# Optimization experiments

Hardware: AMD Instinct MI355X
Metric: run time of the kernel (lower is better)

## Reference

```python
import jax, jax.numpy as jnp
import numpy as np

N_SLOTS = 524288
DIM_MEM = 128
DIM_IN = 1024
SHIFT_RADIUS = 3
EPS = 1e-8  # torch cosine_similarity eps


def setup_inputs() -> dict:
    key = jax.random.key(0)
    k1, k2, k3, k4, k5 = jax.random.split(key, 5)
    n_factors = DIM_MEM + 1 + 1 + (2 * SHIFT_RADIUS + 1) + 1  # 138
    return {
        "input_from_controller": jax.random.normal(k1, (DIM_IN,), dtype=jnp.float32),
        "previous_weighting": jax.random.uniform(k2, (N_SLOTS,), dtype=jnp.float32),
        "memory": jax.random.normal(k3, (N_SLOTS, DIM_MEM), dtype=jnp.float32),
        "W_wf": jax.random.normal(k4, (DIM_IN, n_factors), dtype=jnp.float32) * 0.02,
        "b_wf": jax.random.normal(k5, (n_factors,), dtype=jnp.float32) * 0.02,
    }


def _get_weighting(input_from_controller, previous_weighting, memory, W_wf, b_wf):
    factors = input_from_controller @ W_wf + b_wf  # [138]
    M = DIM_MEM
    key_v = factors[:M]                       # [M]
    key_s = factors[M]                        # scalar (beta)
    gate = jax.nn.softmax(factors[M + 1:M + 2])      # size-1 softmax -> 1.0 (faithful)
    shift_w = jax.nn.softmax(factors[M + 2:M + 2 + 2 * SHIFT_RADIUS + 1])  # [2r+1]
    sharpening = jax.nn.relu(factors[-1]) + 1.0

    # content addressing: cosine similarity of each memory row with key_v
    mem_norm = jnp.maximum(jnp.linalg.norm(memory, axis=1), EPS)  # [N]
    key_norm = jnp.maximum(jnp.linalg.norm(key_v), EPS)
    content_w = (memory @ key_v) / (mem_norm * key_norm)          # [N]
    content_w = jax.nn.softmax(key_s * content_w)

    gated_w = content_w * gate[0] + (1.0 - gate[0]) * previous_weighting

    # circular convolution: shifted[i] = sum_j gated[(i - r + j) % N] * shift_w[j]
    shifted_w = jnp.zeros_like(gated_w)
    for j in range(2 * SHIFT_RADIUS + 1):  # small fixed tap count (7)
        shifted_w = shifted_w + shift_w[j] * jnp.roll(gated_w, SHIFT_RADIUS - j)

    pw = shifted_w ** sharpening
    return pw / pw.sum()


def reference(input_from_controller, previous_weighting, memory, W_wf, b_wf):
    w = _get_weighting(input_from_controller, previous_weighting, memory, W_wf, b_wf)
    read_vector = w @ memory  # read head forward
    return read_vector
```

## Files before the change

kernel.cpp:

```cpp
#include <hip/hip_runtime.h>
#include <math.h>

#define N_SLOTS 524288
#define DIM_MEM 128
#define DIM_IN 1024
#define NFACT 138
#define EPSF 1e-8f


__global__ __launch_bounds__(256) void k_factors(const float* __restrict__ x,
                                                 const float* __restrict__ W,
                                                 const float* __restrict__ b,
                                                 float* __restrict__ factors) {
    int j = threadIdx.x;
    int i0 = blockIdx.x * 32;
    if (j < NFACT) {
        float acc = 0.f;
        #pragma unroll 8
        for (int i = i0; i < i0 + 32; ++i)
            acc = fmaf(x[i], W[(size_t)i * NFACT + j], acc);
        if (blockIdx.x == 0) acc += b[j];
        atomicAdd(&factors[j], acc);
    }
}

__global__ void k_derived(const float* __restrict__ f, float* __restrict__ d) {
    int l = threadIdx.x;
    float v = f[l] * f[l] + f[l + 64] * f[l + 64];
    for (int off = 32; off; off >>= 1) v += __shfl_xor(v, off, 64);
    if (l == 0) {
        float key_norm = fmaxf(sqrtf(v), EPSF);
        float key_s = f[128];
        d[0] = key_s / key_norm;
        float m = f[130];
        for (int j = 1; j < 7; ++j) m = fmaxf(m, f[130 + j]);
        float e[7], s = 0.f;
        for (int j = 0; j < 7; ++j) { e[j] = expf(f[130 + j] - m); s += e[j]; }
        for (int j = 0; j < 7; ++j) d[1 + j] = e[j] / s;
        d[8] = fmaxf(f[137], 0.f) + 1.f;
    }
}

__global__ __launch_bounds__(256) void k_content(const float* __restrict__ mem,
                                                 const float* __restrict__ keyv,
                                                 const float* __restrict__ der,
                                                 float* __restrict__ e_out,
                                                 double* __restrict__ S_acc) {
    __shared__ float s_sum;
    if (threadIdx.x == 0) s_sum = 0.f;
    __syncthreads();
    const int lane = threadIdx.x & 31;
    const int hw   = threadIdx.x >> 5;
    const float4 k4 = ((const float4*)keyv)[lane];
    const float d0 = der[0];
    float local = 0.f;
    const int stride = gridDim.x * 8;
    for (int r = blockIdx.x * 8 + hw; r < N_SLOTS; r += stride) {
        float4 m4 = ((const float4*)(mem + (size_t)r * DIM_MEM))[lane];
        float dot = m4.x * k4.x + m4.y * k4.y + m4.z * k4.z + m4.w * k4.w;
        float n2  = m4.x * m4.x + m4.y * m4.y + m4.z * m4.z + m4.w * m4.w;
        for (int off = 16; off; off >>= 1) {
            dot += __shfl_xor(dot, off, 32);
            n2  += __shfl_xor(n2,  off, 32);
        }
        if (lane == 0) {
            float score = d0 * dot / fmaxf(sqrtf(n2), EPSF);
            float e = expf(score);
            e_out[r] = e;
            local += e;
        }
    }
    if (lane == 0) atomicAdd(&s_sum, local);
    __syncthreads();
    if (threadIdx.x == 0) atomicAdd(S_acc, (double)s_sum);
}

__global__ __launch_bounds__(256) void k_shift(const float* __restrict__ e,
                                               const float* __restrict__ der,
                                               const double* __restrict__ S_acc,
                                               float* __restrict__ p_out,
                                               double* __restrict__ P_acc) {
    __shared__ float s_sum;
    if (threadIdx.x == 0) s_sum = 0.f;
    __syncthreads();
    const int i = blockIdx.x * blockDim.x + threadIdx.x;
    const float invS = (float)(1.0 / *S_acc);
    const float sh = der[8];
    float t = 0.f;
    #pragma unroll
    for (int d = 0; d < 7; ++d) {
        int idx = i + d - 3;
        if (idx < 0) idx += N_SLOTS;
        if (idx >= N_SLOTS) idx -= N_SLOTS;
        t = fmaf(der[1 + d], e[idx], t);
    }
    float p = powf(t * invS, sh);
    p_out[i] = p;
    float w = p;
    for (int off = 32; off; off >>= 1) w += __shfl_xor(w, off, 64);
    if ((threadIdx.x & 63) == 0) atomicAdd(&s_sum, w);
    __syncthreads();
    if (threadIdx.x == 0) atomicAdd(P_acc, (double)s_sum);
}

__global__ __launch_bounds__(256) void k_read(const float* __restrict__ mem,
                                              const float* __restrict__ p,
                                              const double* __restrict__ P_acc,
                                              float* __restrict__ out) {
    __shared__ float partials[8][DIM_MEM];
    const int lane = threadIdx.x & 31;
    const int hw   = threadIdx.x >> 5;
    const float invP = (float)(1.0 / *P_acc);
    float4 acc = make_float4(0.f, 0.f, 0.f, 0.f);
    const int stride = gridDim.x * 8;
    for (int r = blockIdx.x * 8 + hw; r < N_SLOTS; r += stride) {
        float w = p[r] * invP;
        float4 m4 = ((const float4*)(mem + (size_t)r * DIM_MEM))[lane];
        acc.x = fmaf(w, m4.x, acc.x);
        acc.y = fmaf(w, m4.y, acc.y);
        acc.z = fmaf(w, m4.z, acc.z);
        acc.w = fmaf(w, m4.w, acc.w);
    }
    ((float4*)partials[hw])[lane] = acc;
    __syncthreads();
    if (threadIdx.x < DIM_MEM) {
        float s = 0.f;
        #pragma unroll
        for (int h = 0; h < 8; ++h) s += partials[h][threadIdx.x];
        atomicAdd(&out[threadIdx.x], s);
    }
}

extern "C" void kernel_launch(void* const* d_in, const int* in_sizes, int n_in,
                              void* d_out, int out_size, void* d_ws, size_t ws_size,
                              hipStream_t stream) {
    const float* x   = (const float*)d_in[0];
    const float* mem = (const float*)d_in[2];
    const float* W   = (const float*)d_in[3];
    const float* b   = (const float*)d_in[4];
    float* out = (float*)d_out;

    char* ws = (char*)d_ws;
    float*  factors = (float*)ws;
    float*  derived = (float*)(ws + 1024);
    double* S_acc   = (double*)(ws + 2048);
    double* P_acc   = (double*)(ws + 2056);
    float*  e_buf   = (float*)(ws + 4096);
    float*  p_buf   = (float*)(ws + 4096 + (size_t)N_SLOTS * 4);

    hipMemsetAsync(ws, 0, 4096, stream);
    hipMemsetAsync(d_out, 0, DIM_MEM * sizeof(float), stream);

    k_factors<<<DIM_IN / 32, 256, 0, stream>>>(x, W, b, factors);
    k_derived<<<1, 64, 0, stream>>>(factors, derived);
    k_content<<<1024, 256, 0, stream>>>(mem, factors, derived, e_buf, S_acc);
    k_shift<<<N_SLOTS / 256, 256, 0, stream>>>(e_buf, derived, S_acc, p_buf, P_acc);
    k_read<<<1024, 256, 0, stream>>>(mem, p_buf, P_acc, out);
}
```

Baseline: 459.2 us.

## Fuse content scoring, circular shift and read into one pass over memory

Replaces the separate content, shift and read kernels with one kernel. Each block loads 64 memory rows into registers once, computes their exponentiated cosine scores into shared memory plus a 3-row halo on each side, applies the 7-tap shift and sharpening, and accumulates the weighted read in the same pass. It drops the softmax normalizer, since it cancels in the final sharpened normalization, and divides the unnormalized numerator by the weight sum in a small final kernel. This removes the second full read of memory and the intermediate e and p buffers. In exchange it recomputes halo rows per block and relies on unnormalized powf values staying in float range.

```diff
diff --git a/kernel.cpp b/kernel.cpp
--- a/kernel.cpp
+++ b/kernel.cpp
@@ -6,6 +6,7 @@
 #define DIM_IN 1024
 #define NFACT 138
 #define EPSF 1e-8f
+#define ROWS_PB 64
 
 
 __global__ __launch_bounds__(256) void k_factors(const float* __restrict__ x,
@@ -30,8 +31,7 @@
     for (int off = 32; off; off >>= 1) v += __shfl_xor(v, off, 64);
     if (l == 0) {
         float key_norm = fmaxf(sqrtf(v), EPSF);
-        float key_s = f[128];
-        d[0] = key_s / key_norm;
+        d[0] = f[128] / key_norm;
         float m = f[130];
         for (int j = 1; j < 7; ++j) m = fmaxf(m, f[130 + j]);
         float e[7], s = 0.f;
@@ -41,94 +41,99 @@
     }
 }
 
-__global__ __launch_bounds__(256) void k_content(const float* __restrict__ mem,
-                                                 const float* __restrict__ keyv,
-                                                 const float* __restrict__ der,
-                                                 float* __restrict__ e_out,
-                                                 double* __restrict__ S_acc) {
-    __shared__ float s_sum;
-    if (threadIdx.x == 0) s_sum = 0.f;
-    __syncthreads();
+__global__ __launch_bounds__(256) void k_main(const float* __restrict__ mem,
+                                              const float* __restrict__ keyv,
+                                              const float* __restrict__ der,
+                                              float* __restrict__ num,
+                                              double* __restrict__ P_acc) {
+    __shared__ float e_sh[ROWS_PB + 6];
+    __shared__ float partials[8][DIM_MEM];
+    __shared__ float psum[8];
     const int lane = threadIdx.x & 31;
     const int hw   = threadIdx.x >> 5;
+    const float4* mem4 = (const float4*)mem;
     const float4 k4 = ((const float4*)keyv)[lane];
     const float d0 = der[0];
-    float local = 0.f;
-    const int stride = gridDim.x * 8;
-    for (int r = blockIdx.x * 8 + hw; r < N_SLOTS; r += stride) {
-        float4 m4 = ((const float4*)(mem + (size_t)r * DIM_MEM))[lane];
-        float dot = m4.x * k4.x + m4.y * k4.y + m4.z * k4.z + m4.w * k4.w;
-        float n2  = m4.x * m4.x + m4.y * m4.y + m4.z * m4.z + m4.w * m4.w;
+    const int r0 = blockIdx.x * ROWS_PB;
+    const int rbase = r0 + hw * 8;
+
+    float4 row[8];
+    #pragma unroll
+    for (int j = 0; j < 8; ++j)
+        row[j] = mem4[(size_t)(rbase + j) * 32 + lane];
+
+    #pragma unroll
+    for (int j = 0; j < 8; ++j) {
+        float dot = row[j].x * k4.x + row[j].y * k4.y + row[j].z * k4.z + row[j].w * k4.w;
+        float n2  = row[j].x * row[j].x + row[j].y * row[j].y + row[j].z * row[j].z + row[j].w * row[j].w;
         for (int off = 16; off; off >>= 1) {
             dot += __shfl_xor(dot, off, 32);
             n2  += __shfl_xor(n2,  off, 32);
         }
-        if (lane == 0) {
-            float score = d0 * dot / fmaxf(sqrtf(n2), EPSF);
-            float e = expf(score);
-            e_out[r] = e;
-            local += e;
+        if (lane == 0)
+            e_sh[3 + hw * 8 + j] = expf(d0 * dot / fmaxf(sqrtf(n2), EPSF));
+    }
+
+    if (hw < 2) {
+        #pragma unroll
+        for (int j = 0; j < 3; ++j) {
+            int r = (hw == 0) ? (r0 - 3 + j + N_SLOTS) % N_SLOTS
+                              : (r0 + ROWS_PB + j) % N_SLOTS;
+            float4 m4 = mem4[(size_t)r * 32 + lane];
+            float dot = m4.x * k4.x + m4.y * k4.y + m4.z * k4.z + m4.w * k4.w;
+            float n2  = m4.x * m4.x + m4.y * m4.y + m4.z * m4.z + m4.w * m4.w;
+            for (int off = 16; off; off >>= 1) {
+                dot += __shfl_xor(dot, off, 32);
+                n2  += __shfl_xor(n2,  off, 32);
+            }
+            if (lane == 0)
+                e_sh[(hw == 0) ? j : (ROWS_PB + 3 + j)] =
+                    expf(d0 * dot / fmaxf(sqrtf(n2), EPSF));
         }
     }
-    if (lane == 0) atomicAdd(&s_sum, local);
     __syncthreads();
-    if (threadIdx.x == 0) atomicAdd(S_acc, (double)s_sum);
-}
 
-__global__ __launch_bounds__(256) void k_shift(const float* __restrict__ e,
-                                               const float* __restrict__ der,
-                                               const double* __restrict__ S_acc,
-                                               float* __restrict__ p_out,
-                                               double* __restrict__ P_acc) {
-    __shared__ float s_sum;
-    if (threadIdx.x == 0) s_sum = 0.f;
-    __syncthreads();
-    const int i = blockIdx.x * blockDim.x + threadIdx.x;
-    const float invS = (float)(1.0 / *S_acc);
-    const float sh = der[8];
-    float t = 0.f;
+    const float sharp = der[8];
+    float sw[7];
     #pragma unroll
-    for (int d = 0; d < 7; ++d) {
-        int idx = i + d - 3;
-        if (idx < 0) idx += N_SLOTS;
-        if (idx >= N_SLOTS) idx -= N_SLOTS;
-        t = fmaf(der[1 + d], e[idx], t);
-    }
-    float p = powf(t * invS, sh);
-    p_out[i] = p;
-    float w = p;
-    for (int off = 32; off; off >>= 1) w += __shfl_xor(w, off, 64);
-    if ((threadIdx.x & 63) == 0) atomicAdd(&s_sum, w);
-    __syncthreads();
-    if (threadIdx.x == 0) atomicAdd(P_acc, (double)s_sum);
-}
-
-__global__ __launch_bounds__(256) void k_read(const float* __restrict__ mem,
-                                              const float* __restrict__ p,
-                                              const double* __restrict__ P_acc,
-                                              float* __restrict__ out) {
-    __shared__ float partials[8][DIM_MEM];
-    const int lane = threadIdx.x & 31;
-    const int hw   = threadIdx.x >> 5;
-    const float invP = (float)(1.0 / *P_acc);
+    for (int d = 0; d < 7; ++d) sw[d] = der[1 + d];
     float4 acc = make_float4(0.f, 0.f, 0.f, 0.f);
-    const int stride = gridDim.x * 8;
-    for (int r = blockIdx.x * 8 + hw; r < N_SLOTS; r += stride) {
-        float w = p[r] * invP;
-        float4 m4 = ((const float4*)(mem + (size_t)r * DIM_MEM))[lane];
-        acc.x = fmaf(w, m4.x, acc.x);
-        acc.y = fmaf(w, m4.y, acc.y);
-        acc.z = fmaf(w, m4.z, acc.z);
-        acc.w = fmaf(w, m4.w, acc.w);
+    float wsum = 0.f;
+    #pragma unroll
+    for (int j = 0; j < 8; ++j) {
+        const int i = hw * 8 + j;
+        float t = 0.f;
+        #pragma unroll
+        for (int d = 0; d < 7; ++d) t = fmaf(sw[d], e_sh[i + d], t);
+        float w = powf(t, sharp);
+        wsum += w;
+        acc.x = fmaf(w, row[j].x, acc.x);
+        acc.y = fmaf(w, row[j].y, acc.y);
+        acc.z = fmaf(w, row[j].z, acc.z);
+        acc.w = fmaf(w, row[j].w, acc.w);
     }
     ((float4*)partials[hw])[lane] = acc;
+    if (lane == 0) psum[hw] = wsum;
     __syncthreads();
+
     if (threadIdx.x < DIM_MEM) {
         float s = 0.f;
         #pragma unroll
         for (int h = 0; h < 8; ++h) s += partials[h][threadIdx.x];
-        atomicAdd(&out[threadIdx.x], s);
+        atomicAdd(&num[threadIdx.x], s);
     }
+    if (threadIdx.x == 0) {
+        float s = 0.f;
+        #pragma unroll
+        for (int h = 1; h < 8; ++h) s += psum[h];
+        atomicAdd(P_acc, (double)(s + psum[0]));
+    }
+}
+
+__global__ void k_final(const float* __restrict__ num,
+                        const double* __restrict__ P_acc,
+                        float* __restrict__ out) {
+    out[threadIdx.x] = num[threadIdx.x] / (float)(*P_acc);
 }
 
 extern "C" void kernel_launch(void* const* d_in, const int* in_sizes, int n_in,
@@ -143,17 +148,13 @@
     char* ws = (char*)d_ws;
     float*  factors = (float*)ws;
     float*  derived = (float*)(ws + 1024);
-    double* S_acc   = (double*)(ws + 2048);
-    double* P_acc   = (double*)(ws + 2056);
-    float*  e_buf   = (float*)(ws + 4096);
-    float*  p_buf   = (float*)(ws + 4096 + (size_t)N_SLOTS * 4);
+    double* P_acc   = (double*)(ws + 2048);
+    float*  num     = (float*)(ws + 2176);
 
     hipMemsetAsync(ws, 0, 4096, stream);
-    hipMemsetAsync(d_out, 0, DIM_MEM * sizeof(float), stream);
 
     k_factors<<<DIM_IN / 32, 256, 0, stream>>>(x, W, b, factors);
     k_derived<<<1, 64, 0, stream>>>(factors, derived);
-    k_content<<<1024, 256, 0, stream>>>(mem, factors, derived, e_buf, S_acc);
-    k_shift<<<N_SLOTS / 256, 256, 0, stream>>>(e_buf, derived, S_acc, p_buf, P_acc);
-    k_read<<<1024, 256, 0, stream>>>(mem, p_buf, P_acc, out);
+    k_main<<<N_SLOTS / ROWS_PB, 256, 0, stream>>>(mem, factors, derived, num, P_acc);
+    k_final<<<1, DIM_MEM, 0, stream>>>(num, P_acc, out);
 }
```

New measurement: 505.3 us. 1.1x slower.
